# Kernel optimization log

Hardware: AMD Instinct MI355X
Metric: run time of the kernel (lower is better)

## Reference

```python
import jax, jax.numpy as jnp
import numpy as np

N_HEADS = 32
N_KV_HEADS = 8
HEAD_DIM = 128
EPS = 1e-6


def _rope_tables(seq_len, dim, base=10000.0):
    inv_freq = 1.0 / (base ** (np.arange(0, dim, 2, dtype=np.float32) / dim))
    t = np.arange(seq_len, dtype=np.float32)
    freqs = np.outer(t, inv_freq)            # [S, d/2]
    emb = np.concatenate([freqs, freqs], -1)  # [S, d]
    return jnp.asarray(np.cos(emb)), jnp.asarray(np.sin(emb))


def setup_inputs() -> dict:
    key = jax.random.key(0)
    ks = jax.random.split(key, 6)
    B, S, H = 1, 2048, 4096
    d = HEAD_DIM
    cos, sin = _rope_tables(S, d)
    return {
        "hidden_states": jax.random.normal(ks[0], (B, S, H), jnp.float32),
        "position_ids": jnp.broadcast_to(jnp.arange(S, dtype=jnp.int64 if jax.config.jax_enable_x64 else jnp.int32), (B, S)),
        "Wq": jax.random.normal(ks[1], (N_HEADS * d, H), jnp.float32) * 0.02,
        "Wk": jax.random.normal(ks[2], (N_KV_HEADS * d, H), jnp.float32) * 0.02,
        "Wv": jax.random.normal(ks[3], (N_KV_HEADS * d, H), jnp.float32) * 0.02,
        "Wo": jax.random.normal(ks[4], (H, N_HEADS * d), jnp.float32) * 0.02,
        "q_norm_w": jnp.ones((d,), jnp.float32),
        "k_norm_w": jnp.ones((d,), jnp.float32),
        "cos": cos,
        "sin": sin,
    }


def _rmsnorm(x, w):
    xf = x.astype(jnp.float32)
    var = jnp.mean(xf * xf, axis=-1, keepdims=True)
    return (w * (xf * jax.lax.rsqrt(var + EPS))).astype(x.dtype)


def _rotate_half(x):
    x1, x2 = jnp.split(x, 2, axis=-1)
    return jnp.concatenate([-x2, x1], axis=-1)


def reference(hidden_states, position_ids, Wq, Wk, Wv, Wo, q_norm_w, k_norm_w, cos, sin):
    B, S, H = hidden_states.shape
    d = HEAD_DIM
    n_rep = N_HEADS // N_KV_HEADS

    # projections -> [B, nH, S, d] / [B, nKV, S, d]
    q = (hidden_states @ Wq.T).reshape(B, S, N_HEADS, d).transpose(0, 2, 1, 3)
    k = (hidden_states @ Wk.T).reshape(B, S, N_KV_HEADS, d).transpose(0, 2, 1, 3)
    v = (hidden_states @ Wv.T).reshape(B, S, N_KV_HEADS, d).transpose(0, 2, 1, 3)

    # per-head QK RMSNorm
    q = _rmsnorm(q, q_norm_w)
    k = _rmsnorm(k, k_norm_w)

    # RoPE: cos/sin gathered by position_ids -> [B, 1, S, d]
    c = cos[position_ids][:, None, :, :]
    s = sin[position_ids][:, None, :, :]
    q = q * c + _rotate_half(q) * s
    k = k * c + _rotate_half(k) * s

    # GQA: repeat kv heads
    k = jnp.repeat(k, n_rep, axis=1)
    v = jnp.repeat(v, n_rep, axis=1)

    # causal SDPA
    scale = 1.0 / jnp.sqrt(jnp.asarray(d, jnp.float32))
    scores = jnp.einsum("bhqd,bhkd->bhqk", q, k) * scale
    causal = jnp.tril(jnp.ones((S, S), bool))
    scores = jnp.where(causal[None, None], scores, jnp.finfo(scores.dtype).min)
    probs = jax.nn.softmax(scores, axis=-1)
    attn = jnp.einsum("bhqk,bhkd->bhqd", probs, v)

    out = attn.transpose(0, 2, 1, 3).reshape(B, S, N_HEADS * d)
    return out @ Wo.T
```

## Files before the change

### kernel.cpp

```cpp
#include <hip/hip_runtime.h>


typedef __attribute__((ext_vector_type(4))) float    f32x4;
typedef __attribute__((ext_vector_type(8))) _Float16 f16x8;
typedef __attribute__((ext_vector_type(4))) _Float16 f16x4;
typedef __attribute__((ext_vector_type(2))) _Float16 f16x2;

#define AS1 __attribute__((address_space(1)))
#define AS3 __attribute__((address_space(3)))

static __device__ __forceinline__ void gld_lds16(const void* g, void* l) {
  __builtin_amdgcn_global_load_lds((AS1 void*)(g), (AS3 void*)(l), 16, 0, 0);
}

static __device__ __forceinline__ void barrier_raw() {
  asm volatile("s_barrier" ::: "memory");
}
#define WAIT_VMCNT(n) asm volatile("s_waitcnt vmcnt(" #n ")" ::: "memory")

__global__ void f32_to_f16(const float* __restrict__ src,
                           _Float16* __restrict__ dst, int n4) {
  int i = blockIdx.x * blockDim.x + threadIdx.x;
  if (i >= n4) return;
  float4 v = ((const float4*)src)[i];
  f16x4 o = {(_Float16)v.x, (_Float16)v.y, (_Float16)v.z, (_Float16)v.w};
  ((f16x4*)dst)[i] = o;
}

template <int BN>
__global__ __launch_bounds__(512, 2) void gemm256(
    const _Float16* __restrict__ A, const _Float16* __restrict__ B,
    float* __restrict__ C, int N, int K) {
  constexpr int NI = BN / 64;
  constexpr int NB = NI / 2;
  __shared__ _Float16 lA[2][256 * 64];
  __shared__ _Float16 lB[2][BN * 64];
  const int tid = threadIdx.x;
  const int lane = tid & 63;
  const int wid = tid >> 6;
  const int quad = lane >> 4, l16 = lane & 15;
  const int wr = wid >> 2, wc = wid & 3;
  const int bid = blockIdx.x;
  const int m0 = (bid & 7) * 256;
  const int n0 = (bid >> 3) * BN;

  const int sr = tid >> 3, sch = tid & 7;
  const int swz = l16 & 7;

  f32x4 acc[8][NI];
#pragma unroll
  for (int i = 0; i < 8; i++)
#pragma unroll
    for (int j = 0; j < NI; j++) acc[i][j] = f32x4{0.f, 0.f, 0.f, 0.f};

  const int nt = K >> 6;

  auto stageA = [&](int bb, int h, int kt) {
#pragma unroll
    for (int u = 0; u < 2; ++u) {
      int rl = u * 64 + sr;
      int r = h * 128 + rl;
      int cg = sch ^ (rl & 7);
      gld_lds16(A + (size_t)(m0 + r) * K + kt * 64 + cg * 8,
                &lA[bb][(size_t)r * 64 + sch * 8]);
    }
  };
  auto stageB = [&](int bb, int h, int kt) {
#pragma unroll
    for (int u = 0; u < 2; ++u) {
      int rl = u * 64 + sr;
      int r = h * 128 + rl;
      int cg = sch ^ (rl & 7);
      gld_lds16(B + (size_t)(n0 + r) * K + kt * 64 + cg * 8,
                &lB[bb][(size_t)r * 64 + sch * 8]);
    }
  };

  auto ldA = [&](f16x8* dst, int qm, int bb) {
#pragma unroll
    for (int mi = 0; mi < 4; ++mi)
#pragma unroll
      for (int kk = 0; kk < 2; ++kk) {
        int row = wr * 128 + (qm * 4 + mi) * 16 + l16;
        int ch = (kk * 4 + quad) ^ swz;
        dst[mi * 2 + kk] = *(const f16x8*)&lA[bb][(size_t)row * 64 + ch * 8];
      }
  };
  auto ldB = [&](f16x8* dst, int qn, int bb) {
#pragma unroll
    for (int ni = 0; ni < NB; ++ni)
#pragma unroll
      for (int kk = 0; kk < 2; ++kk) {
        int row = wc * (BN / 4) + (qn * NB + ni) * 16 + l16;
        int ch = (kk * 4 + quad) ^ swz;
        dst[ni * 2 + kk] = *(const f16x8*)&lB[bb][(size_t)row * 64 + ch * 8];
      }
  };
  auto mmQ = [&](const f16x8* af, const f16x8* bf, int qm, int qn) {
    __builtin_amdgcn_s_setprio(1);
    __builtin_amdgcn_sched_barrier(0);
#pragma unroll
    for (int mi = 0; mi < 4; ++mi)
#pragma unroll
      for (int ni = 0; ni < NB; ++ni)
#pragma unroll
        for (int kk = 0; kk < 2; ++kk)
          acc[qm * 4 + mi][qn * NB + ni] =
              __builtin_amdgcn_mfma_f32_16x16x32_f16(
                  af[mi * 2 + kk], bf[ni * 2 + kk],
                  acc[qm * 4 + mi][qn * NB + ni], 0, 0, 0);
    __builtin_amdgcn_sched_barrier(0);
    __builtin_amdgcn_s_setprio(0);
  };

  stageA(0, 0, 0);
  stageA(0, 1, 0);
  stageB(0, 0, 0);
  if constexpr (BN == 256) stageB(0, 1, 0);
  stageB(1, 0, 1);
  if constexpr (BN == 256) stageB(1, 1, 1);
  if constexpr (BN == 256) {
    WAIT_VMCNT(4);
  } else {
    WAIT_VMCNT(2);
  }
  barrier_raw();

  f16x8 af[8], b0[2 * NB], b1[2 * NB];
  for (int t = 0; t < nt; ++t) {
    const int b = t & 1;
    const int tn1 = (t + 1 < nt) ? t + 1 : t;
    const int tn2 = (t + 2 < nt) ? t + 2 : t;
    ldA(af, 0, b);
    ldB(b0, 0, b);
    stageA(b ^ 1, 0, tn1);
    barrier_raw();
    mmQ(af, b0, 0, 0);
    barrier_raw();
    ldB(b1, 1, b);
    stageA(b ^ 1, 1, tn1);
    barrier_raw();
    mmQ(af, b1, 0, 1);
    barrier_raw();
    ldA(af, 1, b);
    stageB(b, 0, tn2);
    barrier_raw();
    mmQ(af, b1, 1, 1);
    barrier_raw();
    if constexpr (BN == 256) stageB(b, 1, tn2);
    if constexpr (BN == 256) {
      WAIT_VMCNT(4);
    } else {
      WAIT_VMCNT(2);
    }
    barrier_raw();
    mmQ(af, b0, 1, 0);
    barrier_raw();
  }

#pragma unroll
  for (int mi8 = 0; mi8 < 8; ++mi8) {
    int m = m0 + wr * 128 + mi8 * 16 + quad * 4;
#pragma unroll
    for (int ni = 0; ni < NI; ++ni) {
      int n = n0 + wc * (BN / 4) + ni * 16 + l16;
      float* cp = C + (size_t)m * N + n;
#pragma unroll
      for (int r = 0; r < 4; ++r) cp[(size_t)r * N] = acc[mi8][ni][r];
    }
  }
}

__global__ void norm_rope(const float* __restrict__ raw, int row_stride,
                          int col_off, const float* __restrict__ w,
                          const float* __restrict__ cosb,
                          const float* __restrict__ sinb,
                          const int* __restrict__ pos,
                          _Float16* __restrict__ out, int nh_log2, int S) {
  int gt = blockIdx.x * blockDim.x + threadIdx.x;
  int wid = gt >> 6, lane = gt & 63;
  int h = wid & ((1 << nh_log2) - 1);
  int s = wid >> nh_log2;
  const float* x = raw + (size_t)s * row_stride + col_off + h * 128;
  float2 v = *(const float2*)&x[lane * 2];
  float ss = v.x * v.x + v.y * v.y;
#pragma unroll
  for (int m = 1; m < 64; m <<= 1) ss += __shfl_xor(ss, m);
  float inv = rsqrtf(ss * (1.f / 128.f) + 1e-6f);
  int p = pos[s];
  float n0 = v.x * inv * w[lane * 2];
  float n1 = v.y * inv * w[lane * 2 + 1];
  float p0 = __shfl_xor(n0, 32);
  float p1 = __shfl_xor(n1, 32);
  float r0 = (lane < 32) ? -p0 : p0;
  float r1 = (lane < 32) ? -p1 : p1;
  float c0 = cosb[p * 128 + lane * 2], c1 = cosb[p * 128 + lane * 2 + 1];
  float s0 = sinb[p * 128 + lane * 2], s1 = sinb[p * 128 + lane * 2 + 1];
  f16x2 o;
  o.x = (_Float16)(n0 * c0 + r0 * s0);
  o.y = (_Float16)(n1 * c1 + r1 * s1);
  *(f16x2*)&out[((size_t)h * S + s) * 128 + lane * 2] = o;
}

__global__ __launch_bounds__(256) void v_trans(const float* __restrict__ vraw,
                                               int row_stride,
                                               _Float16* __restrict__ vt,
                                               int S) {
  __shared__ _Float16 tile[64][72];
  int s0 = blockIdx.x * 64, c0 = blockIdx.y * 64;
  int t = threadIdx.x;
  int r = t >> 2, cq = (t & 3) * 16;
  const float* src = vraw + (size_t)(s0 + r) * row_stride + c0 + cq;
#pragma unroll
  for (int j = 0; j < 4; j++) {
    float4 v = *(const float4*)&src[j * 4];
    tile[r][cq + j * 4 + 0] = (_Float16)v.x;
    tile[r][cq + j * 4 + 1] = (_Float16)v.y;
    tile[r][cq + j * 4 + 2] = (_Float16)v.z;
    tile[r][cq + j * 4 + 3] = (_Float16)v.w;
  }
  __syncthreads();
  int orow = t >> 2, sq = (t & 3) * 16;
  _Float16* dst = vt + (size_t)(c0 + orow) * S + s0 + sq;
  f16x8 a, b;
#pragma unroll
  for (int j = 0; j < 8; j++) a[j] = tile[sq + j][orow];
#pragma unroll
  for (int j = 0; j < 8; j++) b[j] = tile[sq + 8 + j][orow];
  *(f16x8*)&dst[0] = a;
  *(f16x8*)&dst[8] = b;
}

__global__ __launch_bounds__(256, 2) void flash_attn(
    const _Float16* __restrict__ Qh, const _Float16* __restrict__ Kh,
    const _Float16* __restrict__ Vt, _Float16* __restrict__ Oout, int S) {
  __shared__ _Float16 lK[2][32 * 128];
  __shared__ _Float16 lV[2][128 * 32];
  __shared__ _Float16 plds[4][16][40];
  const int wave = threadIdx.x >> 6, lane = threadIdx.x & 63;
  const int quad = lane >> 4, l16 = lane & 15;

  const int flat = blockIdx.y * gridDim.x + blockIdx.x;
  const int head = (flat & 7) * 4 + ((flat >> 3) & 3);
  const int px   = flat >> 5;
  const int kvh  = head >> 2;
  const _Float16* K = Kh + (size_t)kvh * S * 128;
  const _Float16* V = Vt + (size_t)kvh * 128 * S;

  const int ksw = l16 & 7;
  const int vchunk = quad ^ ((l16 >> 1) & 3);
  const float scale = 0.08838834764831845f;
  const float Mc = 5.0f;

#pragma unroll
  for (int seg = 0; seg < 2; ++seg) {
    const int tile = seg ? (31 - px) : px;
    const int q0 = tile * 64;
    const int wq = q0 + wave * 16;
    const _Float16* Q = Qh + ((size_t)head * S + wq) * 128;

    f16x8 qf[4];
#pragma unroll
    for (int kq = 0; kq < 4; kq++)
      qf[kq] = *(const f16x8*)&Q[(size_t)l16 * 128 + kq * 32 + quad * 8];

    f32x4 o[8];
#pragma unroll
    for (int t = 0; t < 8; t++) o[t] = f32x4{0.f, 0.f, 0.f, 0.f};
    float l_i = 0.f;
    const int q_row = wq + l16;
    const int ktend = 2 * tile + 1;

#pragma unroll
    for (int u = 0; u < 2; ++u) {
      int j = wave * 2 + u;
      int rK = j * 4 + (lane >> 4);
      int cK = (lane & 15) ^ (rK & 7);
      gld_lds16(K + (size_t)rK * 128 + cK * 8, &lK[0][j * 512]);
      int rV = j * 16 + (lane >> 2);
      int cV = (lane & 3) ^ ((rV >> 1) & 3);
      gld_lds16(V + (size_t)rV * S + cV * 8, &lV[0][j * 512]);
    }
    __builtin_amdgcn_s_waitcnt(0);
    __syncthreads();

    int cur = 0;
    for (int kt = 0; kt <= ktend; ++kt) {
      if (kt < ktend) {
        const int kn = (kt + 1) * 32;
#pragma unroll
        for (int u = 0; u < 2; ++u) {
          int j = wave * 2 + u;
          int rK = j * 4 + (lane >> 4);
          int cK = (lane & 15) ^ (rK & 7);
          gld_lds16(K + (size_t)(kn + rK) * 128 + cK * 8, &lK[cur ^ 1][j * 512]);
          int rV = j * 16 + (lane >> 2);
          int cV = (lane & 3) ^ ((rV >> 1) & 3);
          gld_lds16(V + (size_t)rV * S + kn + cV * 8, &lV[cur ^ 1][j * 512]);
        }
      }
      if (kt * 32 <= wq + 15) {
        f32x4 sc[2];
        sc[0] = f32x4{0.f, 0.f, 0.f, 0.f};
        sc[1] = f32x4{0.f, 0.f, 0.f, 0.f};
#pragma unroll
        for (int mt = 0; mt < 2; mt++)
#pragma unroll
          for (int kq = 0; kq < 4; kq++) {
            f16x8 kf = *(const f16x8*)&lK[cur][(mt * 16 + l16) * 128 +
                                              (((kq * 4 + quad) ^ ksw) * 8)];
            sc[mt] = __builtin_amdgcn_mfma_f32_16x16x32_f16(kf, qf[kq], sc[mt],
                                                            0, 0, 0);
          }
        float p[2][4];
        float rsum = 0.f;
#pragma unroll
        for (int mt = 0; mt < 2; mt++)
#pragma unroll
          for (int r = 0; r < 4; r++) {
            int kcol = kt * 32 + mt * 16 + quad * 4 + r;
            float e = __expf(fmaf(sc[mt][r], scale, -Mc));
            e = (kcol <= q_row) ? e : 0.f;
            p[mt][r] = e;
            rsum += e;
          }
        rsum += __shfl_xor(rsum, 16);
        rsum += __shfl_xor(rsum, 32);
        l_i += rsum;
        f16x4 pk0 = {(_Float16)p[0][0], (_Float16)p[0][1], (_Float16)p[0][2],
                     (_Float16)p[0][3]};
        f16x4 pk1 = {(_Float16)p[1][0], (_Float16)p[1][1], (_Float16)p[1][2],
                     (_Float16)p[1][3]};
        *(f16x4*)&plds[wave][l16][quad * 4] = pk0;
        *(f16x4*)&plds[wave][l16][16 + quad * 4] = pk1;
        f16x8 pf = *(const f16x8*)&plds[wave][l16][quad * 8];
#pragma unroll
        for (int t = 0; t < 8; t++) {
          f16x8 vf = *(const f16x8*)&lV[cur][(t * 16 + l16) * 32 + vchunk * 8];
          o[t] = __builtin_amdgcn_mfma_f32_16x16x32_f16(vf, pf, o[t], 0, 0, 0);
        }
      }
      __builtin_amdgcn_s_waitcnt(0);
      __syncthreads();
      cur ^= 1;
    }

    const float invl = 1.f / l_i;
    _Float16* op = Oout + (size_t)q_row * 4096 + head * 128 + quad * 4;
#pragma unroll
    for (int t = 0; t < 8; t++) {
      f16x4 ov = {(_Float16)(o[t][0] * invl), (_Float16)(o[t][1] * invl),
                  (_Float16)(o[t][2] * invl), (_Float16)(o[t][3] * invl)};
      *(f16x4*)&op[t * 16] = ov;
    }
  }
}

extern "C" void kernel_launch(void* const* d_in, const int* in_sizes, int n_in,
                              void* d_out, int out_size, void* d_ws,
                              size_t ws_size, hipStream_t stream) {
  const int S = 2048, H = 4096, NH = 32, NKV = 8, D = 128;
  const int NQKV = NH * D + 2 * NKV * D;
  const float* hs   = (const float*)d_in[0];
  const int*   pos  = (const int*)d_in[1];
  const float* Wq   = (const float*)d_in[2];
  const float* Wk   = (const float*)d_in[3];
  const float* Wv   = (const float*)d_in[4];
  const float* Wo   = (const float*)d_in[5];
  const float* qw   = (const float*)d_in[6];
  const float* kw   = (const float*)d_in[7];
  const float* cosb = (const float*)d_in[8];
  const float* sinb = (const float*)d_in[9];
  float* out = (float*)d_out;

  char* ws = (char*)d_ws;
  _Float16* wqkv    = (_Float16*)(ws + 0);
  _Float16* hid_bf  = (_Float16*)(ws + 50331648);
  float*    qkv_raw = (float*)(ws + 67108864);
  _Float16* q_bf    = (_Float16*)(ws + 117440512);
  _Float16* k_bf    = (_Float16*)(ws + 134217728);
  _Float16* v_t     = (_Float16*)(ws + 138412032);
  _Float16* attn_bf = (_Float16*)(ws + 67108864);
  _Float16* wo_bf   = (_Float16*)(ws + 0);

  f32_to_f16<<<(S * H / 4 + 255) / 256, 256, 0, stream>>>(hs, hid_bf, S * H / 4);
  f32_to_f16<<<(H * H / 4 + 255) / 256, 256, 0, stream>>>(Wq, wqkv, H * H / 4);
  f32_to_f16<<<(NKV * D * H / 4 + 255) / 256, 256, 0, stream>>>(
      Wk, wqkv + (size_t)H * H, NKV * D * H / 4);
  f32_to_f16<<<(NKV * D * H / 4 + 255) / 256, 256, 0, stream>>>(
      Wv, wqkv + (size_t)(H + NKV * D) * H, NKV * D * H / 4);

  gemm256<256><<<dim3((NQKV / 256) * 8), 512, 0, stream>>>(hid_bf, wqkv,
                                                           qkv_raw, NQKV, H);
  f32_to_f16<<<(H * H / 4 + 255) / 256, 256, 0, stream>>>(Wo, wo_bf, H * H / 4);

  norm_rope<<<S * NH / 4, 256, 0, stream>>>(qkv_raw, NQKV, 0, qw, cosb, sinb,
                                            pos, q_bf, 5, S);
  norm_rope<<<S * NKV / 4, 256, 0, stream>>>(qkv_raw, NQKV, H, kw, cosb, sinb,
                                             pos, k_bf, 3, S);
  v_trans<<<dim3(S / 64, NKV * D / 64), 256, 0, stream>>>(
      qkv_raw + (size_t)(H + NKV * D), NQKV, v_t, S);

  flash_attn<<<dim3(16, NH), 256, 0, stream>>>(q_bf, k_bf, v_t, attn_bf, S);

  gemm256<128><<<dim3((H / 128) * 8), 512, 0, stream>>>(attn_bf, wo_bf, out, H,
                                                        H);
}
```

Baseline: 528.4 us.

## Fuse input conversions, store QKV in fp16, triple-buffer flash attention K/V

Merges the four fp32-to-fp16 conversion launches into one kernel. The QKV GEMM now writes fp16 instead of fp32, which halves that intermediate's write and read traffic for norm_rope and v_trans. Flash attention moves from double to triple buffering of its K/V tiles, prefetching two tiles ahead with partial vmcnt waits so loads overlap compute. The fp16 intermediate adds rounding before the RMSNorm, and the third buffer raises LDS use, which may limit occupancy.

```diff
diff --git a/kernel.cpp b/kernel.cpp
--- a/kernel.cpp
+++ b/kernel.cpp
@@ -27,10 +27,35 @@
   ((f16x4*)dst)[i] = o;
 }
 
-template <int BN>
+__global__ void cvt4(const float* __restrict__ s0, const float* __restrict__ s1,
+                     const float* __restrict__ s2, const float* __restrict__ s3,
+                     _Float16* __restrict__ d0, _Float16* __restrict__ d1,
+                     _Float16* __restrict__ d2, _Float16* __restrict__ d3,
+                     int n0, int n1, int n2, int n3) {
+  int i = blockIdx.x * blockDim.x + threadIdx.x;
+  const float* s;
+  _Float16* d;
+  int j = i;
+  if (j < n0) {
+    s = s0; d = d0;
+  } else if ((j -= n0) < n1) {
+    s = s1; d = d1;
+  } else if ((j -= n1) < n2) {
+    s = s2; d = d2;
+  } else if ((j -= n2) < n3) {
+    s = s3; d = d3;
+  } else {
+    return;
+  }
+  float4 v = ((const float4*)s)[j];
+  f16x4 o = {(_Float16)v.x, (_Float16)v.y, (_Float16)v.z, (_Float16)v.w};
+  ((f16x4*)d)[j] = o;
+}
+
+template <int BN, typename CT>
 __global__ __launch_bounds__(512, 2) void gemm256(
     const _Float16* __restrict__ A, const _Float16* __restrict__ B,
-    float* __restrict__ C, int N, int K) {
+    CT* __restrict__ C, int N, int K) {
   constexpr int NI = BN / 64;
   constexpr int NB = NI / 2;
   __shared__ _Float16 lA[2][256 * 64];
@@ -164,14 +189,14 @@
 #pragma unroll
     for (int ni = 0; ni < NI; ++ni) {
       int n = n0 + wc * (BN / 4) + ni * 16 + l16;
-      float* cp = C + (size_t)m * N + n;
-#pragma unroll
-      for (int r = 0; r < 4; ++r) cp[(size_t)r * N] = acc[mi8][ni][r];
-    }
-  }
-}
-
-__global__ void norm_rope(const float* __restrict__ raw, int row_stride,
+      CT* cp = C + (size_t)m * N + n;
+#pragma unroll
+      for (int r = 0; r < 4; ++r) cp[(size_t)r * N] = (CT)acc[mi8][ni][r];
+    }
+  }
+}
+
+__global__ void norm_rope(const _Float16* __restrict__ raw, int row_stride,
                           int col_off, const float* __restrict__ w,
                           const float* __restrict__ cosb,
                           const float* __restrict__ sinb,
@@ -181,15 +206,16 @@
   int wid = gt >> 6, lane = gt & 63;
   int h = wid & ((1 << nh_log2) - 1);
   int s = wid >> nh_log2;
-  const float* x = raw + (size_t)s * row_stride + col_off + h * 128;
-  float2 v = *(const float2*)&x[lane * 2];
-  float ss = v.x * v.x + v.y * v.y;
+  const _Float16* x = raw + (size_t)s * row_stride + col_off + h * 128;
+  f16x2 v2 = *(const f16x2*)&x[lane * 2];
+  float vx = (float)v2.x, vy = (float)v2.y;
+  float ss = vx * vx + vy * vy;
 #pragma unroll
   for (int m = 1; m < 64; m <<= 1) ss += __shfl_xor(ss, m);
   float inv = rsqrtf(ss * (1.f / 128.f) + 1e-6f);
   int p = pos[s];
-  float n0 = v.x * inv * w[lane * 2];
-  float n1 = v.y * inv * w[lane * 2 + 1];
+  float n0 = vx * inv * w[lane * 2];
+  float n1 = vy * inv * w[lane * 2 + 1];
   float p0 = __shfl_xor(n0, 32);
   float p1 = __shfl_xor(n1, 32);
   float r0 = (lane < 32) ? -p0 : p0;
@@ -202,7 +228,7 @@
   *(f16x2*)&out[((size_t)h * S + s) * 128 + lane * 2] = o;
 }
 
-__global__ __launch_bounds__(256) void v_trans(const float* __restrict__ vraw,
+__global__ __launch_bounds__(256) void v_trans(const _Float16* __restrict__ vraw,
                                                int row_stride,
                                                _Float16* __restrict__ vt,
                                                int S) {
@@ -210,14 +236,13 @@
   int s0 = blockIdx.x * 64, c0 = blockIdx.y * 64;
   int t = threadIdx.x;
   int r = t >> 2, cq = (t & 3) * 16;
-  const float* src = vraw + (size_t)(s0 + r) * row_stride + c0 + cq;
-#pragma unroll
-  for (int j = 0; j < 4; j++) {
-    float4 v = *(const float4*)&src[j * 4];
-    tile[r][cq + j * 4 + 0] = (_Float16)v.x;
-    tile[r][cq + j * 4 + 1] = (_Float16)v.y;
-    tile[r][cq + j * 4 + 2] = (_Float16)v.z;
-    tile[r][cq + j * 4 + 3] = (_Float16)v.w;
+  const _Float16* src = vraw + (size_t)(s0 + r) * row_stride + c0 + cq;
+  f16x8 u0 = *(const f16x8*)&src[0];
+  f16x8 u1 = *(const f16x8*)&src[8];
+#pragma unroll
+  for (int j = 0; j < 8; j++) {
+    tile[r][cq + j] = u0[j];
+    tile[r][cq + 8 + j] = u1[j];
   }
   __syncthreads();
   int orow = t >> 2, sq = (t & 3) * 16;
@@ -234,8 +259,8 @@
 __global__ __launch_bounds__(256, 2) void flash_attn(
     const _Float16* __restrict__ Qh, const _Float16* __restrict__ Kh,
     const _Float16* __restrict__ Vt, _Float16* __restrict__ Oout, int S) {
-  __shared__ _Float16 lK[2][32 * 128];
-  __shared__ _Float16 lV[2][128 * 32];
+  __shared__ _Float16 lK[3][32 * 128];
+  __shared__ _Float16 lV[3][128 * 32];
   __shared__ _Float16 plds[4][16][40];
   const int wave = threadIdx.x >> 6, lane = threadIdx.x & 63;
   const int quad = lane >> 4, l16 = lane & 15;
@@ -252,6 +277,19 @@
   const float scale = 0.08838834764831845f;
   const float Mc = 5.0f;
 
+  auto stage = [&](int kt, int bi) {
+#pragma unroll
+    for (int u = 0; u < 2; ++u) {
+      int j = wave * 2 + u;
+      int rK = j * 4 + (lane >> 4);
+      int cK = (lane & 15) ^ (rK & 7);
+      gld_lds16(K + (size_t)(kt * 32 + rK) * 128 + cK * 8, &lK[bi][j * 512]);
+      int rV = j * 16 + (lane >> 2);
+      int cV = (lane & 3) ^ ((rV >> 1) & 3);
+      gld_lds16(V + (size_t)rV * S + kt * 32 + cV * 8, &lV[bi][j * 512]);
+    }
+  };
+
 #pragma unroll
   for (int seg = 0; seg < 2; ++seg) {
     const int tile = seg ? (31 - px) : px;
@@ -271,34 +309,15 @@
     const int q_row = wq + l16;
     const int ktend = 2 * tile + 1;
 
-#pragma unroll
-    for (int u = 0; u < 2; ++u) {
-      int j = wave * 2 + u;
-      int rK = j * 4 + (lane >> 4);
-      int cK = (lane & 15) ^ (rK & 7);
-      gld_lds16(K + (size_t)rK * 128 + cK * 8, &lK[0][j * 512]);
-      int rV = j * 16 + (lane >> 2);
-      int cV = (lane & 3) ^ ((rV >> 1) & 3);
-      gld_lds16(V + (size_t)rV * S + cV * 8, &lV[0][j * 512]);
-    }
-    __builtin_amdgcn_s_waitcnt(0);
-    __syncthreads();
-
-    int cur = 0;
+    stage(0, 0);
+    stage(1, 1);
+    WAIT_VMCNT(4);
+    barrier_raw();
+
     for (int kt = 0; kt <= ktend; ++kt) {
-      if (kt < ktend) {
-        const int kn = (kt + 1) * 32;
-#pragma unroll
-        for (int u = 0; u < 2; ++u) {
-          int j = wave * 2 + u;
-          int rK = j * 4 + (lane >> 4);
-          int cK = (lane & 15) ^ (rK & 7);
-          gld_lds16(K + (size_t)(kn + rK) * 128 + cK * 8, &lK[cur ^ 1][j * 512]);
-          int rV = j * 16 + (lane >> 2);
-          int cV = (lane & 3) ^ ((rV >> 1) & 3);
-          gld_lds16(V + (size_t)rV * S + kn + cV * 8, &lV[cur ^ 1][j * 512]);
-        }
-      }
+      const int cur = kt % 3;
+      const bool more = (kt + 2 <= ktend);
+      if (more) stage(kt + 2, (kt + 2) % 3);
       if (kt * 32 <= wq + 15) {
         f32x4 sc[2];
         sc[0] = f32x4{0.f, 0.f, 0.f, 0.f};
@@ -340,9 +359,12 @@
           o[t] = __builtin_amdgcn_mfma_f32_16x16x32_f16(vf, pf, o[t], 0, 0, 0);
         }
       }
-      __builtin_amdgcn_s_waitcnt(0);
-      __syncthreads();
-      cur ^= 1;
+      if (more) {
+        WAIT_VMCNT(4);
+      } else {
+        WAIT_VMCNT(0);
+      }
+      barrier_raw();
     }
 
     const float invl = 1.f / l_i;
@@ -376,33 +398,35 @@
   char* ws = (char*)d_ws;
   _Float16* wqkv    = (_Float16*)(ws + 0);
   _Float16* hid_bf  = (_Float16*)(ws + 50331648);
-  float*    qkv_raw = (float*)(ws + 67108864);
+  _Float16* qkv_f16 = (_Float16*)(ws + 67108864);
   _Float16* q_bf    = (_Float16*)(ws + 117440512);
   _Float16* k_bf    = (_Float16*)(ws + 134217728);
   _Float16* v_t     = (_Float16*)(ws + 138412032);
-  _Float16* attn_bf = (_Float16*)(ws + 67108864);
+  _Float16* attn_bf = (_Float16*)(ws + 96468992);
   _Float16* wo_bf   = (_Float16*)(ws + 0);
 
-  f32_to_f16<<<(S * H / 4 + 255) / 256, 256, 0, stream>>>(hs, hid_bf, S * H / 4);
-  f32_to_f16<<<(H * H / 4 + 255) / 256, 256, 0, stream>>>(Wq, wqkv, H * H / 4);
-  f32_to_f16<<<(NKV * D * H / 4 + 255) / 256, 256, 0, stream>>>(
-      Wk, wqkv + (size_t)H * H, NKV * D * H / 4);
-  f32_to_f16<<<(NKV * D * H / 4 + 255) / 256, 256, 0, stream>>>(
-      Wv, wqkv + (size_t)(H + NKV * D) * H, NKV * D * H / 4);
-
-  gemm256<256><<<dim3((NQKV / 256) * 8), 512, 0, stream>>>(hid_bf, wqkv,
-                                                           qkv_raw, NQKV, H);
+  const int n_hs4 = S * H / 4;
+  const int n_wq4 = NH * D * H / 4;
+  const int n_wk4 = NKV * D * H / 4;
+  const int n_wv4 = NKV * D * H / 4;
+  const int ncvt = n_hs4 + n_wq4 + n_wk4 + n_wv4;
+  cvt4<<<(ncvt + 255) / 256, 256, 0, stream>>>(
+      hs, Wq, Wk, Wv, hid_bf, wqkv, wqkv + (size_t)H * H,
+      wqkv + (size_t)(H + NKV * D) * H, n_hs4, n_wq4, n_wk4, n_wv4);
+
+  gemm256<256, _Float16><<<dim3((NQKV / 256) * 8), 512, 0, stream>>>(
+      hid_bf, wqkv, qkv_f16, NQKV, H);
   f32_to_f16<<<(H * H / 4 + 255) / 256, 256, 0, stream>>>(Wo, wo_bf, H * H / 4);
 
-  norm_rope<<<S * NH / 4, 256, 0, stream>>>(qkv_raw, NQKV, 0, qw, cosb, sinb,
+  norm_rope<<<S * NH / 4, 256, 0, stream>>>(qkv_f16, NQKV, 0, qw, cosb, sinb,
                                             pos, q_bf, 5, S);
-  norm_rope<<<S * NKV / 4, 256, 0, stream>>>(qkv_raw, NQKV, H, kw, cosb, sinb,
+  norm_rope<<<S * NKV / 4, 256, 0, stream>>>(qkv_f16, NQKV, H, kw, cosb, sinb,
                                              pos, k_bf, 3, S);
   v_trans<<<dim3(S / 64, NKV * D / 64), 256, 0, stream>>>(
-      qkv_raw + (size_t)(H + NKV * D), NQKV, v_t, S);
+      qkv_f16 + (size_t)(H + NKV * D), NQKV, v_t, S);
 
   flash_attn<<<dim3(16, NH), 256, 0, stream>>>(q_bf, k_bf, v_t, attn_bf, S);
 
-  gemm256<128><<<dim3((H / 128) * 8), 512, 0, stream>>>(attn_bf, wo_bf, out, H,
-                                                        H);
-}
+  gemm256<128, float><<<dim3((H / 128) * 8), 512, 0, stream>>>(attn_bf, wo_bf,
+                                                               out, H, H);
+}
```

Result: no change. 522.5 us (-1.1%).
